# Kernel optimization log

Measured on AMD Instinct MI355X. Metric: run time of the kernel, lower is better.

The kernel has to match this reference:

```python
import jax, jax.numpy as jnp
import numpy as np


def setup_inputs() -> dict:
    key = jax.random.key(0)
    k1, k2 = jax.random.split(key)
    N, C, H, W = 2, 128, 256, 256
    k, m = 7, 8
    feat = jax.random.normal(k1, (N, C, H, W), dtype=jnp.float32)
    filters_lr = jax.random.normal(k2, (N, C * k * k, H // m, W // m), dtype=jnp.float32)
    return {"feat": feat, "filters_lr": filters_lr, "kernel_size": k, "block_size": m}


def _block_fac(feat, filters_lr, k, m):
    # feat: [N,C,H,W]; filters_lr: [N, C*k^2, H/m, W/m]
    N, C, H, W = feat.shape
    Hb, Wb = H // m, W // m
    k2 = k * k
    pad = (k - 1) // 2
    # weight_permute_reshape: NCHW -> NHWC -> [N,Hb,Wb,C,k2] (C slowest, then tap)
    w = jnp.transpose(filters_lr, (0, 2, 3, 1)).reshape(N, Hb, Wb, C, k2)
    x = jnp.transpose(feat, (0, 2, 3, 1))  # NHWC
    xp = jnp.pad(x, ((0, 0), (pad, pad), (pad, pad), (0, 0)))
    out = jnp.zeros_like(x)
    # tap index t = dh*k + dw (matches torch unfold(2,k) then unfold(3,k) ordering)
    for t in range(k2):
        dh, dw = t // k, t % k
        # per-block weight for this tap, upsampled to full resolution: [N,H,W,C]
        w_t = jnp.repeat(jnp.repeat(w[..., t], m, axis=1), m, axis=2)
        out = out + xp[:, dh:dh + H, dw:dw + W, :] * w_t
    return jnp.transpose(out, (0, 3, 1, 2))  # back to NCHW


def reference(feat, filters_lr, kernel_size, block_size):
    return _block_fac(feat, filters_lr, kernel_size, block_size)
```

## Files before the change

### kernel.cpp

```cpp
#include <hip/hip_runtime.h>
#include <stdint.h>


#define SLABF 1568

typedef const uint32_t __attribute__((address_space(1))) guint;
typedef uint32_t __attribute__((address_space(3))) luint;

__global__ __launch_bounds__(256, 1)
void block_fac_kernel(const float* __restrict__ feat,
                      const float* __restrict__ filt,
                      float* __restrict__ out) {
    __shared__ float s_w[4 * SLABF];

    const int wave = threadIdx.x >> 6;
    const int lane = threadIdx.x & 63;
    const int wid  = (blockIdx.x << 2) | wave;
    const int hb   = wid & 31;
    const int c    = (wid >> 5) & 127;
    const int n    = wid >> 12;

    const int c0 = lane << 2;
    const int wb = lane >> 1;
    const int H0 = hb * 8;

    const float* fbase = feat + (size_t)(n * 128 + c) * (256 * 256);
    const float* wtap  = filt + (size_t)((n * 128 + c) * 49) * 1024 + hb * 32;
    float* slab = s_w + wave * SLABF;

    #pragma unroll
    for (int i = 0; i < 7; ++i) {
        if (i < 6 || lane < 8) {
            int f = (i << 6) | lane;
            const float* gp = wtap + (size_t)(f >> 3) * 1024 + (f & 7) * 4;
            float* lp = slab + i * 256;
            __builtin_amdgcn_global_load_lds((guint*)gp, (luint*)lp, 16, 0, 0);
        }
    }

    float4 row[14];
    #pragma unroll
    for (int r = 0; r < 14; ++r) {
        int gr  = H0 - 3 + r;
        int grc = gr < 0 ? 0 : (gr > 255 ? 255 : gr);
        row[r] = *(const float4*)(fbase + (size_t)grc * 256 + c0);
    }

    asm volatile("s_waitcnt vmcnt(0)" ::: "memory");
    __builtin_amdgcn_sched_barrier(0);

    const float* ws = slab + wb;
    float wt[49];
    #pragma unroll
    for (int t = 0; t < 49; ++t) wt[t] = ws[t * 32];

    const int addrL = ((lane - 1) & 63) << 2;
    const int addrR = ((lane + 1) & 63) << 2;
    const bool l0  = (lane == 0);
    const bool l63 = (lane == 63);

    float acc[8][4] = {};

    #pragma unroll
    for (int jj = 0; jj < 14; ++jj) {
        const int gr = H0 - 3 + jj;
        float4 f = row[jj];
        if (gr < 0 || gr > 255) f = make_float4(0.f, 0.f, 0.f, 0.f);

        float L1 = __int_as_float(__builtin_amdgcn_ds_bpermute(addrL, __float_as_int(f.y)));
        float L2 = __int_as_float(__builtin_amdgcn_ds_bpermute(addrL, __float_as_int(f.z)));
        float L3 = __int_as_float(__builtin_amdgcn_ds_bpermute(addrL, __float_as_int(f.w)));
        float R0 = __int_as_float(__builtin_amdgcn_ds_bpermute(addrR, __float_as_int(f.x)));
        float R1 = __int_as_float(__builtin_amdgcn_ds_bpermute(addrR, __float_as_int(f.y)));
        float R2 = __int_as_float(__builtin_amdgcn_ds_bpermute(addrR, __float_as_int(f.z)));
        if (l0)  { L1 = 0.f; L2 = 0.f; L3 = 0.f; }
        if (l63) { R0 = 0.f; R1 = 0.f; R2 = 0.f; }

        float win[12] = {0.f, L1, L2, L3,
                         f.x, f.y, f.z, f.w,
                         R0, R1, R2, 0.f};
        #pragma unroll
        for (int a = 0; a < 8; ++a) {
            int dh = jj - a;
            if (dh >= 0 && dh <= 6) {
                #pragma unroll
                for (int dw = 0; dw < 7; ++dw) {
                    float wv = wt[dh * 7 + dw];
                    #pragma unroll
                    for (int i = 0; i < 4; ++i)
                        acc[a][i] += win[i + dw + 1] * wv;
                }
            }
        }
    }

    float* obase = out + (size_t)((n * 128 + c) * 256 + H0) * 256 + c0;
    #pragma unroll
    for (int a = 0; a < 8; ++a)
        *(float4*)(obase + (size_t)(a * 256)) =
            make_float4(acc[a][0], acc[a][1], acc[a][2], acc[a][3]);
}

extern "C" void kernel_launch(void* const* d_in, const int* in_sizes, int n_in,
                              void* d_out, int out_size, void* d_ws, size_t ws_size,
                              hipStream_t stream) {
    const float* feat = (const float*)d_in[0];
    const float* filt = (const float*)d_in[1];
    float* out = (float*)d_out;
    dim3 grid(2 * 128 * 32 / 4);
    dim3 block(256);
    hipLaunchKernelGGL(block_fac_kernel, grid, block, 0, stream, feat, filt, out);
}
```

Before: 40.60 us.

## Make each wave process four row-blocks with double-buffered LDS weight prefetch

Each block is now a single 64-thread wave that loops over four consecutive 8-row blocks of one channel, instead of four waves each handling one row block. The filter slab for the next row block is prefetched into a second LDS buffer via global_load_lds while the current one is computed, and the feature rows are loaded per iteration. This aims to hide weight-load latency and cut LDS use per block. In exchange it launches a quarter as many waves, which reduces the parallelism available to hide memory latency in a bandwidth-bound kernel. The vmcnt(0) wait at the top of each iteration also serialises on the previous iteration's stores.

```diff
diff --git a/kernel.cpp b/kernel.cpp
--- a/kernel.cpp
+++ b/kernel.cpp
@@ -7,98 +7,112 @@
 typedef const uint32_t __attribute__((address_space(1))) guint;
 typedef uint32_t __attribute__((address_space(3))) luint;
 
-__global__ __launch_bounds__(256, 1)
+__global__ __launch_bounds__(64, 3)
 void block_fac_kernel(const float* __restrict__ feat,
                       const float* __restrict__ filt,
                       float* __restrict__ out) {
-    __shared__ float s_w[4 * SLABF];
+    __shared__ float s_w[2 * SLABF];
 
-    const int wave = threadIdx.x >> 6;
-    const int lane = threadIdx.x & 63;
-    const int wid  = (blockIdx.x << 2) | wave;
-    const int hb   = wid & 31;
-    const int c    = (wid >> 5) & 127;
-    const int n    = wid >> 12;
+    const int bid = blockIdx.x;
+    const int q   = bid & 7;
+    const int c   = (bid >> 3) & 127;
+    const int n   = bid >> 10;
+    const int lane = threadIdx.x;
 
     const int c0 = lane << 2;
     const int wb = lane >> 1;
-    const int H0 = hb * 8;
 
-    const float* fbase = feat + (size_t)(n * 128 + c) * (256 * 256);
-    const float* wtap  = filt + (size_t)((n * 128 + c) * 49) * 1024 + hb * 32;
-    float* slab = s_w + wave * SLABF;
+    const float* fbase = feat + (size_t)(n * 128 + c) * 65536;
+    const float* wtap0 = filt + (size_t)((n * 128 + c) * 49) * 1024 + q * 128;
 
     #pragma unroll
     for (int i = 0; i < 7; ++i) {
         if (i < 6 || lane < 8) {
             int f = (i << 6) | lane;
-            const float* gp = wtap + (size_t)(f >> 3) * 1024 + (f & 7) * 4;
-            float* lp = slab + i * 256;
-            __builtin_amdgcn_global_load_lds((guint*)gp, (luint*)lp, 16, 0, 0);
+            const float* gp = wtap0 + (size_t)(f >> 3) * 1024 + (f & 7) * 4;
+            __builtin_amdgcn_global_load_lds((guint*)gp, (luint*)(s_w + i * 256), 16, 0, 0);
         }
     }
-
-    float4 row[14];
-    #pragma unroll
-    for (int r = 0; r < 14; ++r) {
-        int gr  = H0 - 3 + r;
-        int grc = gr < 0 ? 0 : (gr > 255 ? 255 : gr);
-        row[r] = *(const float4*)(fbase + (size_t)grc * 256 + c0);
-    }
-
-    asm volatile("s_waitcnt vmcnt(0)" ::: "memory");
-    __builtin_amdgcn_sched_barrier(0);
-
-    const float* ws = slab + wb;
-    float wt[49];
-    #pragma unroll
-    for (int t = 0; t < 49; ++t) wt[t] = ws[t * 32];
 
     const int addrL = ((lane - 1) & 63) << 2;
     const int addrR = ((lane + 1) & 63) << 2;
     const bool l0  = (lane == 0);
     const bool l63 = (lane == 63);
 
-    float acc[8][4] = {};
+    #pragma unroll 1
+    for (int t = 0; t < 4; ++t) {
+        asm volatile("s_waitcnt vmcnt(0)" ::: "memory");
+        __builtin_amdgcn_sched_barrier(0);
 
-    #pragma unroll
-    for (int jj = 0; jj < 14; ++jj) {
-        const int gr = H0 - 3 + jj;
-        float4 f = row[jj];
-        if (gr < 0 || gr > 255) f = make_float4(0.f, 0.f, 0.f, 0.f);
+        const float* ws = s_w + ((t & 1) ? SLABF : 0) + wb;
+        float wt[49];
+        #pragma unroll
+        for (int k = 0; k < 49; ++k) wt[k] = ws[k * 32];
 
-        float L1 = __int_as_float(__builtin_amdgcn_ds_bpermute(addrL, __float_as_int(f.y)));
-        float L2 = __int_as_float(__builtin_amdgcn_ds_bpermute(addrL, __float_as_int(f.z)));
-        float L3 = __int_as_float(__builtin_amdgcn_ds_bpermute(addrL, __float_as_int(f.w)));
-        float R0 = __int_as_float(__builtin_amdgcn_ds_bpermute(addrR, __float_as_int(f.x)));
-        float R1 = __int_as_float(__builtin_amdgcn_ds_bpermute(addrR, __float_as_int(f.y)));
-        float R2 = __int_as_float(__builtin_amdgcn_ds_bpermute(addrR, __float_as_int(f.z)));
-        if (l0)  { L1 = 0.f; L2 = 0.f; L3 = 0.f; }
-        if (l63) { R0 = 0.f; R1 = 0.f; R2 = 0.f; }
+        const int H0 = (q * 4 + t) * 8;
 
-        float win[12] = {0.f, L1, L2, L3,
-                         f.x, f.y, f.z, f.w,
-                         R0, R1, R2, 0.f};
+        float4 row[14];
         #pragma unroll
-        for (int a = 0; a < 8; ++a) {
-            int dh = jj - a;
-            if (dh >= 0 && dh <= 6) {
-                #pragma unroll
-                for (int dw = 0; dw < 7; ++dw) {
-                    float wv = wt[dh * 7 + dw];
-                    #pragma unroll
-                    for (int i = 0; i < 4; ++i)
-                        acc[a][i] += win[i + dw + 1] * wv;
+        for (int r = 0; r < 14; ++r) {
+            int gr  = H0 - 3 + r;
+            int grc = gr < 0 ? 0 : (gr > 255 ? 255 : gr);
+            row[r] = *(const float4*)(fbase + (size_t)grc * 256 + c0);
+        }
+
+        if (t < 3) {
+            const float* wtap = wtap0 + (t + 1) * 32;
+            float* dst = s_w + ((t & 1) ? 0 : SLABF);
+            #pragma unroll
+            for (int i = 0; i < 7; ++i) {
+                if (i < 6 || lane < 8) {
+                    int f = (i << 6) | lane;
+                    const float* gp = wtap + (size_t)(f >> 3) * 1024 + (f & 7) * 4;
+                    __builtin_amdgcn_global_load_lds((guint*)gp, (luint*)(dst + i * 256), 16, 0, 0);
                 }
             }
         }
+
+        float acc[8][4] = {};
+
+        #pragma unroll
+        for (int jj = 0; jj < 14; ++jj) {
+            const int gr = H0 - 3 + jj;
+            float4 f = row[jj];
+            if (gr < 0 || gr > 255) f = make_float4(0.f, 0.f, 0.f, 0.f);
+
+            float L1 = __int_as_float(__builtin_amdgcn_ds_bpermute(addrL, __float_as_int(f.y)));
+            float L2 = __int_as_float(__builtin_amdgcn_ds_bpermute(addrL, __float_as_int(f.z)));
+            float L3 = __int_as_float(__builtin_amdgcn_ds_bpermute(addrL, __float_as_int(f.w)));
+            float R0 = __int_as_float(__builtin_amdgcn_ds_bpermute(addrR, __float_as_int(f.x)));
+            float R1 = __int_as_float(__builtin_amdgcn_ds_bpermute(addrR, __float_as_int(f.y)));
+            float R2 = __int_as_float(__builtin_amdgcn_ds_bpermute(addrR, __float_as_int(f.z)));
+            if (l0)  { L1 = 0.f; L2 = 0.f; L3 = 0.f; }
+            if (l63) { R0 = 0.f; R1 = 0.f; R2 = 0.f; }
+
+            float win[12] = {0.f, L1, L2, L3,
+                             f.x, f.y, f.z, f.w,
+                             R0, R1, R2, 0.f};
+            #pragma unroll
+            for (int a = 0; a < 8; ++a) {
+                int dh = jj - a;
+                if (dh >= 0 && dh <= 6) {
+                    #pragma unroll
+                    for (int dw = 0; dw < 7; ++dw) {
+                        float wv = wt[dh * 7 + dw];
+                        #pragma unroll
+                        for (int i = 0; i < 4; ++i)
+                            acc[a][i] += win[i + dw + 1] * wv;
+                    }
+                }
+            }
+        }
+
+        float* obase = out + (size_t)((n * 128 + c) * 256 + H0) * 256 + c0;
+        #pragma unroll
+        for (int a = 0; a < 8; ++a)
+            *(float4*)(obase + (size_t)(a * 256)) =
+                make_float4(acc[a][0], acc[a][1], acc[a][2], acc[a][3]);
     }
-
-    float* obase = out + (size_t)((n * 128 + c) * 256 + H0) * 256 + c0;
-    #pragma unroll
-    for (int a = 0; a < 8; ++a)
-        *(float4*)(obase + (size_t)(a * 256)) =
-            make_float4(acc[a][0], acc[a][1], acc[a][2], acc[a][3]);
 }
 
 extern "C" void kernel_launch(void* const* d_in, const int* in_sizes, int n_in,
@@ -107,7 +121,7 @@
     const float* feat = (const float*)d_in[0];
     const float* filt = (const float*)d_in[1];
     float* out = (float*)d_out;
-    dim3 grid(2 * 128 * 32 / 4);
-    dim3 block(256);
+    dim3 grid(2 * 128 * 8);
+    dim3 block(64);
     hipLaunchKernelGGL(block_fac_kernel, grid, block, 0, stream, feat, filt, out);
 }
```

Result: slower. 71.56 us (+76.3%).
